# Kernel tuning notes

Hardware: AMD Instinct MI355X
Metric: run time of the kernel (lower is better)

## Reference

```python
import jax, jax.numpy as jnp
import numpy as np

THRESHOLD = 0.5
NEG_POS_RATIO = 3
ALPHA = 1.0


def cxcy_to_xy(c):
    # (cx,cy,w,h) -> (xmin,ymin,xmax,ymax)
    return jnp.concatenate([c[..., :2] - c[..., 2:] / 2.0,
                            c[..., :2] + c[..., 2:] / 2.0], axis=-1)


def gcxgcy_to_cxcy(g, priors):
    # standard SSD decode with variances (10, 5)
    return jnp.concatenate([g[..., :2] * priors[..., 2:] / 10.0 + priors[..., :2],
                            jnp.exp(g[..., 2:] / 5.0) * priors[..., 2:]], axis=-1)


def jaccard(set1, set2):
    # set1: [n1,4], set2: [n2,4], xyxy -> IoU matrix [n1,n2]
    lo = jnp.maximum(set1[:, None, :2], set2[None, :, :2])
    hi = jnp.minimum(set1[:, None, 2:], set2[None, :, 2:])
    wh = jnp.clip(hi - lo, 0.0)
    inter = wh[..., 0] * wh[..., 1]
    a1 = (set1[:, 2] - set1[:, 0]) * (set1[:, 3] - set1[:, 1])
    a2 = (set2[:, 2] - set2[:, 0]) * (set2[:, 3] - set2[:, 1])
    return inter / (a1[:, None] + a2[None, :] - inter)


def match_one(b, l, priors_xy):
    # b: [n_obj,4] GT boxes, l: [n_obj] labels, priors_xy: [P,4]
    n_obj = b.shape[0]
    ov = jaccard(b, priors_xy)                      # [n_obj, P]
    obj_for_prior = jnp.argmax(ov, axis=0)          # [P]
    ov_for_prior = jnp.max(ov, axis=0)              # [P]
    prior_for_obj = jnp.argmax(ov, axis=1)          # [n_obj]
    # force each object to own its best prior
    obj_for_prior = obj_for_prior.at[prior_for_obj].set(jnp.arange(n_obj))
    ov_for_prior = ov_for_prior.at[prior_for_obj].set(1.0)
    lab = l[obj_for_prior]
    lab = jnp.where(ov_for_prior < THRESHOLD, 0, lab)
    return lab, b[obj_for_prior]


def ciou(b1, b2):
    # elementwise CIoU over [..., 4] xyxy boxes -> [...]
    w1 = b1[..., 2] - b1[..., 0]; h1 = b1[..., 3] - b1[..., 1]
    w2 = b2[..., 2] - b2[..., 0]; h2 = b2[..., 3] - b2[..., 1]
    area1 = w1 * h1; area2 = w2 * h2
    cx1 = (b1[..., 2] + b1[..., 0]) / 2; cy1 = (b1[..., 3] + b1[..., 1]) / 2
    cx2 = (b2[..., 2] + b2[..., 0]) / 2; cy2 = (b2[..., 3] + b2[..., 1]) / 2
    in_wh = jnp.clip(jnp.minimum(b1[..., 2:], b2[..., 2:]) - jnp.maximum(b1[..., :2], b2[..., :2]), 0.0)
    out_wh = jnp.clip(jnp.maximum(b1[..., 2:], b2[..., 2:]) - jnp.minimum(b1[..., :2], b2[..., :2]), 0.0)
    inner_diag = (cx2 - cx1) ** 2 + (cy2 - cy1) ** 2
    outer_diag = out_wh[..., 0] ** 2 + out_wh[..., 1] ** 2
    inner = in_wh[..., 0] * in_wh[..., 1]
    iou = inner / (area1 + area2 - inner)
    v = (4.0 / (np.pi ** 2)) * (jnp.arctan(w2 / h2) - jnp.arctan(w1 / h1)) ** 2
    alpha = jax.lax.stop_gradient(v / (1.0 - iou + v))  # torch.no_grad()
    return 1.0 - iou + inner_diag / outer_diag + alpha * v


def setup_inputs() -> dict:
    key = jax.random.key(0)
    ks = jax.random.split(key, 7)
    N, P, C, NOBJ = 32, 8732, 81, 24
    predicted_locs = jax.random.normal(ks[0], (N, P, 4), jnp.float32)
    predicted_scores = jax.random.normal(ks[1], (N, P, C), jnp.float32)
    mins = jax.random.uniform(ks[2], (N, NOBJ, 2), minval=0.0, maxval=0.7)
    sizes = jax.random.uniform(ks[3], (N, NOBJ, 2), minval=0.05, maxval=0.3)
    boxes = jnp.concatenate([mins, mins + sizes], axis=-1)  # well-formed xyxy
    labels = jax.random.randint(ks[4], (N, NOBJ), 1, C)      # 1..C-1 (0 = background)
    pc = jax.random.uniform(ks[5], (P, 2), minval=0.05, maxval=0.95)
    pwh = jax.random.uniform(ks[6], (P, 2), minval=0.05, maxval=0.5)
    priors_cxcy = jnp.concatenate([pc, pwh], axis=-1)
    return {"predicted_locs": predicted_locs, "predicted_scores": predicted_scores,
            "boxes": boxes, "labels": labels, "priors_cxcy": priors_cxcy}


def reference(predicted_locs, predicted_scores, boxes, labels, priors_cxcy):
    priors_xy = cxcy_to_xy(priors_cxcy)
    # per-image GT->prior matching (vectorized over batch)
    true_classes, decoded_true = jax.vmap(match_one, in_axes=(0, 0, None))(boxes, labels, priors_xy)
    decoded_pred = cxcy_to_xy(gcxgcy_to_cxcy(predicted_locs, priors_cxcy[None]))  # [N,P,4]
    pos = true_classes != 0                              # [N,P]
    posf = pos.astype(predicted_locs.dtype)
    n_pos_total = jnp.sum(posf)
    # localization: CIoU mean over positive priors
    loc_loss = jnp.sum(ciou(decoded_pred, decoded_true) * posf) / n_pos_total
    # confidence: CE per prior
    logp = jax.nn.log_softmax(predicted_scores, axis=-1)
    conf_all = -jnp.take_along_axis(logp, true_classes[..., None], axis=-1)[..., 0]  # [N,P]
    conf_pos_sum = jnp.sum(conf_all * posf)
    # hard negative mining: top (neg_pos_ratio * n_pos) negatives per image
    conf_neg = jnp.where(pos, 0.0, conf_all)
    conf_neg_sorted = -jnp.sort(-conf_neg, axis=1)       # descending
    n_hard = NEG_POS_RATIO * jnp.sum(pos, axis=1)        # [N]
    ranks = jnp.arange(conf_neg_sorted.shape[1])[None, :]
    hard_mask = (ranks < n_hard[:, None]).astype(conf_all.dtype)
    conf_hard_neg_sum = jnp.sum(conf_neg_sorted * hard_mask)
    conf_loss = (conf_hard_neg_sum + conf_pos_sum) / n_pos_total
    return conf_loss + ALPHA * loc_loss
```

## Files before the change

### kernel.cpp

```cpp
#include <hip/hip_runtime.h>
#include <math.h>

#define BLK  256
#define BLKM 1024

constexpr int N_IMG = 32;
constexpr int P_PRI = 8732;
constexpr int C_CLS = 81;
constexpr int N_OBJ = 24;
constexpr int RPB   = 64;
constexpr int PB2   = (P_PRI + RPB - 1) / RPB;
constexpr int NBLK2 = PB2 * N_IMG;
constexpr int LROW  = 84;
constexpr int NLD   = 6;

__global__ void k_obj_match(const float* __restrict__ boxes,
                            const float* __restrict__ priors,
                            int* __restrict__ prior_for_obj,
                            int* __restrict__ npos) {
    const int o = blockIdx.x;
    const int n = blockIdx.y;
    const int tid = threadIdx.x;

    if (o == 0 && tid == 0) npos[n] = 0;

    const float x1 = boxes[(n * N_OBJ + o) * 4 + 0];
    const float y1 = boxes[(n * N_OBJ + o) * 4 + 1];
    const float x2 = boxes[(n * N_OBJ + o) * 4 + 2];
    const float y2 = boxes[(n * N_OBJ + o) * 4 + 3];
    const float ab = (x2 - x1) * (y2 - y1);

    const float4* pr4 = (const float4*)priors;

    float bv = -1.0f;
    int   bi = P_PRI;
    for (int p = tid; p < P_PRI; p += BLK) {
        const float4 c = pr4[p];
        const float px1 = c.x - c.z / 2.0f, py1 = c.y - c.w / 2.0f;
        const float px2 = c.x + c.z / 2.0f, py2 = c.y + c.w / 2.0f;
        const float pa  = (px2 - px1) * (py2 - py1);
        const float lox = fmaxf(x1, px1), loy = fmaxf(y1, py1);
        const float hix = fminf(x2, px2), hiy = fminf(y2, py2);
        const float iw = fmaxf(hix - lox, 0.0f), ih = fmaxf(hiy - loy, 0.0f);
        const float inter = iw * ih;
        const float iou = inter / (ab + pa - inter);
        if (iou > bv) { bv = iou; bi = p; }
    }

    __shared__ float sv[BLK];
    __shared__ int   si[BLK];
    sv[tid] = bv; si[tid] = bi;
    __syncthreads();
    for (int s = BLK / 2; s > 0; s >>= 1) {
        if (tid < s) {
            const float v2 = sv[tid + s]; const int i2 = si[tid + s];
            if (v2 > sv[tid] || (v2 == sv[tid] && i2 < si[tid])) { sv[tid] = v2; si[tid] = i2; }
        }
        __syncthreads();
    }
    if (tid == 0) prior_for_obj[n * N_OBJ + o] = si[0];
}

__global__ void __launch_bounds__(BLK, 7)
k_main(const float* __restrict__ locs,
       const float* __restrict__ scores,
       const float* __restrict__ boxes,
       const int*   __restrict__ labels,
       const float* __restrict__ priors,
       const int*   __restrict__ prior_for_obj,
       float* __restrict__ conf_neg,
       int*   __restrict__ npos,
       float* __restrict__ partial_conf,
       float* __restrict__ partial_loc) {
    __shared__ float sdata[RPB * LROW];
    __shared__ int   pfo[N_OBJ];
    __shared__ int   slab[N_OBJ];
    __shared__ float wred[4][4];

    const int n   = blockIdx.y;
    const int r0  = blockIdx.x * RPB;
    const int tid = threadIdx.x;
    const int rows = min(RPB, P_PRI - r0);
    const int nvec = (rows * C_CLS) >> 2;

    const float4* src = (const float4*)(scores + ((size_t)n * P_PRI + r0) * C_CLS);
    float4 ld[NLD];
#pragma unroll
    for (int k = 0; k < NLD; ++k) {
        const int i = tid + k * BLK;
        if (i < nvec) ld[k] = src[i];
    }

    if (tid < N_OBJ) pfo[tid] = prior_for_obj[n * N_OBJ + tid];
    if (tid >= 64 && tid < 64 + N_OBJ) slab[tid - 64] = labels[n * N_OBJ + (tid - 64)];

    const int row = tid >> 2;
    const int q   = tid & 3;
    const int p   = r0 + row;
    const int psafe = (p < P_PRI) ? p : (P_PRI - 1);
    const float4 c = ((const float4*)priors)[psafe];
    const float px1 = c.x - c.z / 2.0f, py1 = c.y - c.w / 2.0f;
    const float px2 = c.x + c.z / 2.0f, py2 = c.y + c.w / 2.0f;
    const float pa  = (px2 - px1) * (py2 - py1);

    const float4* bxg = (const float4*)(boxes + (size_t)n * N_OBJ * 4);
    float bv = -1.0f;
    int   bo = q * 6;
#pragma unroll
    for (int j = 0; j < 6; ++j) {
        const int o = q * 6 + j;
        const float4 b = bxg[o];
        const float lox = fmaxf(b.x, px1), loy = fmaxf(b.y, py1);
        const float hix = fminf(b.z, px2), hiy = fminf(b.w, py2);
        const float iw = fmaxf(hix - lox, 0.0f), ih = fmaxf(hiy - loy, 0.0f);
        const float inter = iw * ih;
        const float ab = (b.z - b.x) * (b.w - b.y);
        const float iou = inter / (ab + pa - inter);
        if (iou > bv) { bv = iou; bo = o; }
    }
#pragma unroll
    for (int m = 1; m < 4; m <<= 1) {
        const float v2 = __shfl_xor(bv, m);
        const int   o2 = __shfl_xor(bo, m);
        if (v2 > bv || (v2 == bv && o2 < bo)) { bv = v2; bo = o2; }
    }

#pragma unroll
    for (int k = 0; k < NLD; ++k) {
        const int i = tid + k * BLK;
        if (i < nvec) {
            const int f  = i * 4;
            const int r  = (int)((unsigned)f / 81u);
            const int cc = f - r * 81;
            const int base = r * LROW + cc;
            const float vv[4] = {ld[k].x, ld[k].y, ld[k].z, ld[k].w};
#pragma unroll
            for (int j = 0; j < 4; ++j) {
                int a = base + j;
                if (cc + j >= 81) a += (LROW - C_CLS);
                sdata[a] = vv[j];
            }
        }
    }
    __syncthreads();

    int fo = -1;
#pragma unroll
    for (int j = 0; j < 6; ++j) {
        const int o = q * 6 + j;
        if (pfo[o] == p) fo = o;
    }
#pragma unroll
    for (int m = 1; m < 4; m <<= 1) fo = max(fo, __shfl_xor(fo, m));

    int   obj = (fo >= 0) ? fo : bo;
    float ov  = (fo >= 0) ? 1.0f : bv;

    float s = 0.0f;
    const float* rbase = sdata + row * LROW;
    if (row < rows) {
        const float4* rv = (const float4*)(rbase + 20 * q);
        float a0 = 0.0f, a1 = 0.0f;
#pragma unroll
        for (int i = 0; i < 5; ++i) {
            const float4 v = rv[i];
            a0 += __expf(v.x) + __expf(v.y);
            a1 += __expf(v.z) + __expf(v.w);
        }
        s = a0 + a1;
        if (q == 3) s += __expf(rbase[80]);
    }
    s += __shfl_xor(s, 1);
    s += __shfl_xor(s, 2);

    int cls = slab[obj];
    if (ov < 0.5f) cls = 0;

    float confpos = 0.0f, locv = 0.0f;
    int   cnt1 = 0;
    if (q == 0 && row < rows) {
        const float conf = __logf(s) - rbase[cls];
        const bool pos = (cls != 0);
        conf_neg[n * P_PRI + p] = pos ? 0.0f : fmaxf(conf, 0.0f);
        if (pos) {
            cnt1 = 1;
            confpos = conf;
            const float4 g = ((const float4*)locs)[(size_t)n * P_PRI + p];
            const float cx = g.x * c.z / 10.0f + c.x;
            const float cy = g.y * c.w / 10.0f + c.y;
            const float w  = expf(g.z / 5.0f) * c.z;
            const float hh = expf(g.w / 5.0f) * c.w;
            const float b1x1 = cx - w / 2.0f, b1y1 = cy - hh / 2.0f;
            const float b1x2 = cx + w / 2.0f, b1y2 = cy + hh / 2.0f;

            const float4 tb = bxg[obj];
            const float w1 = b1x2 - b1x1, h1 = b1y2 - b1y1;
            const float w2 = tb.z - tb.x, h2 = tb.w - tb.y;
            const float area1 = w1 * h1,  area2 = w2 * h2;
            const float c1x = (b1x2 + b1x1) / 2.0f, c1y = (b1y2 + b1y1) / 2.0f;
            const float c2x = (tb.z + tb.x) / 2.0f, c2y = (tb.w + tb.y) / 2.0f;
            const float inw = fmaxf(fminf(b1x2, tb.z) - fmaxf(b1x1, tb.x), 0.0f);
            const float inh = fmaxf(fminf(b1y2, tb.w) - fmaxf(b1y1, tb.y), 0.0f);
            const float owd = fmaxf(fmaxf(b1x2, tb.z) - fminf(b1x1, tb.x), 0.0f);
            const float ohd = fmaxf(fmaxf(b1y2, tb.w) - fminf(b1y1, tb.y), 0.0f);
            const float inner_diag = (c2x - c1x) * (c2x - c1x) + (c2y - c1y) * (c2y - c1y);
            const float outer_diag = owd * owd + ohd * ohd;
            const float inner = inw * inh;
            const float iou = inner / (area1 + area2 - inner);
            const float K = 0.40528473456935108577551785283891f;
            const float dat = atanf(w2 / h2) - atanf(w1 / h1);
            const float v = K * dat * dat;
            const float alpha = v / (1.0f - iou + v);
            locv = 1.0f - iou + inner_diag / outer_diag + alpha * v;
        }
    }

#pragma unroll
    for (int off = 32; off > 0; off >>= 1) {
        confpos += __shfl_down(confpos, off);
        locv    += __shfl_down(locv, off);
        cnt1    += __shfl_down(cnt1, off);
    }
    const int wid = tid >> 6;
    if ((tid & 63) == 0) {
        wred[wid][0] = confpos; wred[wid][1] = locv; wred[wid][2] = (float)cnt1;
    }
    __syncthreads();
    if (tid == 0) {
        float a = 0.0f, b = 0.0f, d = 0.0f;
#pragma unroll
        for (int w2 = 0; w2 < 4; ++w2) { a += wred[w2][0]; b += wred[w2][1]; d += wred[w2][2]; }
        const int slot = n * gridDim.x + blockIdx.x;
        partial_conf[slot] = a;
        partial_loc [slot] = b;
        atomicAdd(&npos[n], (int)d);
    }
}

__global__ void __launch_bounds__(BLKM)
k_mine(const float* __restrict__ conf_neg,
       const int*   __restrict__ npos,
       float* __restrict__ hardneg) {
    __shared__ int   wcnt[2][BLKM / 64];
    __shared__ float wsum[BLKM / 64];

    const int n    = blockIdx.x;
    const int tid  = threadIdx.x;
    const int wid  = tid >> 6;
    const int lane = tid & 63;

    unsigned v[9];
#pragma unroll
    for (int k = 0; k < 9; ++k) {
        const int p = tid + k * BLKM;
        v[k] = (p < P_PRI) ? __float_as_uint(conf_neg[n * P_PRI + p]) : 0u;
    }

    int k0 = 3 * npos[n];
    if (k0 > P_PRI) k0 = P_PRI;
    if (k0 <= 0) { if (tid == 0) hardneg[n] = 0.0f; return; }

    unsigned prefix = 0u;
    int kk = k0;
    for (int bit = 30; bit >= 0; --bit) {
        const unsigned hi = (prefix >> bit) | 1u;
        int cnt = 0;
#pragma unroll
        for (int k = 0; k < 9; ++k)
            cnt += __popcll(__ballot((v[k] >> bit) == hi));
        if (lane == 0) wcnt[bit & 1][wid] = cnt;
        __syncthreads();
        int tot = 0;
#pragma unroll
        for (int w = 0; w < BLKM / 64; ++w) tot += wcnt[bit & 1][w];
        if (tot >= kk) prefix |= (1u << bit);
        else           kk -= tot;
    }

    float psum = 0.0f; int pcnt = 0;
#pragma unroll
    for (int k = 0; k < 9; ++k) {
        if (v[k] > prefix) { psum += __uint_as_float(v[k]); ++pcnt; }
    }
#pragma unroll
    for (int off = 32; off > 0; off >>= 1) {
        psum += __shfl_down(psum, off);
        pcnt += __shfl_down(pcnt, off);
    }
    __syncthreads();
    if (lane == 0) { wsum[wid] = psum; wcnt[0][wid] = pcnt; }
    __syncthreads();
    if (tid == 0) {
        float S = 0.0f; int C = 0;
#pragma unroll
        for (int w = 0; w < BLKM / 64; ++w) { S += wsum[w]; C += wcnt[0][w]; }
        hardneg[n] = S + (float)(k0 - C) * __uint_as_float(prefix);
    }
}

__global__ void k_final(const float* __restrict__ partial_conf,
                        const float* __restrict__ partial_loc,
                        const int*   __restrict__ npos,
                        const float* __restrict__ hardneg,
                        float* __restrict__ out) {
    __shared__ float s1[BLK], s2[BLK], s3[BLK];
    __shared__ int   si[BLK];
    const int tid = threadIdx.x;

    float c = 0.0f, l = 0.0f, h = 0.0f;
    int np = 0;
    for (int i = tid; i < NBLK2; i += BLK) { c += partial_conf[i]; l += partial_loc[i]; }
    if (tid < N_IMG) { h = hardneg[tid]; np = npos[tid]; }

    s1[tid] = c; s2[tid] = l; s3[tid] = h; si[tid] = np;
    __syncthreads();
    for (int s = BLK / 2; s > 0; s >>= 1) {
        if (tid < s) { s1[tid] += s1[tid + s]; s2[tid] += s2[tid + s];
                       s3[tid] += s3[tid + s]; si[tid] += si[tid + s]; }
        __syncthreads();
    }
    if (tid == 0) {
        const float npt = (float)si[0];
        const float conf_loss = (s3[0] + s1[0]) / npt;
        const float loc_loss  = s2[0] / npt;
        out[0] = conf_loss + loc_loss;
    }
}

extern "C" void kernel_launch(void* const* d_in, const int* in_sizes, int n_in,
                              void* d_out, int out_size, void* d_ws, size_t ws_size,
                              hipStream_t stream) {
    const float* locs   = (const float*)d_in[0];
    const float* scores = (const float*)d_in[1];
    const float* boxes  = (const float*)d_in[2];
    const int*   labels = (const int*)  d_in[3];
    const float* priors = (const float*)d_in[4];
    float* out = (float*)d_out;

    char* w = (char*)d_ws;
    float* conf_neg      = (float*)w; w += (size_t)N_IMG * P_PRI * 4;
    int*   prior_for_obj = (int*)w;   w += (size_t)N_IMG * N_OBJ * 4;
    int*   npos          = (int*)w;   w += (size_t)N_IMG * 4;
    float* partial_conf  = (float*)w; w += (size_t)NBLK2 * 4;
    float* partial_loc   = (float*)w; w += (size_t)NBLK2 * 4;
    float* hardneg       = (float*)w; w += (size_t)N_IMG * 4;

    dim3 gridO(N_OBJ, N_IMG);
    k_obj_match<<<gridO, BLK, 0, stream>>>(boxes, priors, prior_for_obj, npos);

    dim3 gridM(PB2, N_IMG);
    k_main<<<gridM, BLK, 0, stream>>>(locs, scores, boxes, labels, priors,
                                      prior_for_obj, conf_neg, npos,
                                      partial_conf, partial_loc);

    k_mine<<<N_IMG, BLKM, 0, stream>>>(conf_neg, npos, hardneg);

    k_final<<<1, BLK, 0, stream>>>(partial_conf, partial_loc, npos, hardneg, out);
}
```

Measured before the change: 88.44 us.

## Load score rows directly into registers with strided per-thread reads, dropping LDS staging

Replaces the coalesced float4 load of the whole score tile into padded shared memory with each thread reading 20 strided scalars (q + 4*i) of its own row straight from global memory. The logit for the target class is now picked in registers with a compare-select and combined across the 4 lanes with shuffles, instead of being read from LDS. This removes the LDS write/read traffic and the 21.5 KB shared allocation, which should allow more resident blocks, and the launch-bounds occupancy hint is relaxed to match. The cost is less efficient global access: adjacent lanes touch interleaved words of 324-byte rows and issue scalar loads rather than vector ones.

```diff
diff --git a/kernel.cpp b/kernel.cpp
--- a/kernel.cpp
+++ b/kernel.cpp
@@ -11,8 +11,6 @@
 constexpr int RPB   = 64;
 constexpr int PB2   = (P_PRI + RPB - 1) / RPB;
 constexpr int NBLK2 = PB2 * N_IMG;
-constexpr int LROW  = 84;
-constexpr int NLD   = 6;
 
 __global__ void k_obj_match(const float* __restrict__ boxes,
                             const float* __restrict__ priors,
@@ -61,7 +59,7 @@
     if (tid == 0) prior_for_obj[n * N_OBJ + o] = si[0];
 }
 
-__global__ void __launch_bounds__(BLK, 7)
+__global__ void __launch_bounds__(BLK)
 k_main(const float* __restrict__ locs,
        const float* __restrict__ scores,
        const float* __restrict__ boxes,
@@ -72,7 +70,6 @@
        int*   __restrict__ npos,
        float* __restrict__ partial_conf,
        float* __restrict__ partial_loc) {
-    __shared__ float sdata[RPB * LROW];
     __shared__ int   pfo[N_OBJ];
     __shared__ int   slab[N_OBJ];
     __shared__ float wred[4][4];
@@ -81,15 +78,6 @@
     const int r0  = blockIdx.x * RPB;
     const int tid = threadIdx.x;
     const int rows = min(RPB, P_PRI - r0);
-    const int nvec = (rows * C_CLS) >> 2;
-
-    const float4* src = (const float4*)(scores + ((size_t)n * P_PRI + r0) * C_CLS);
-    float4 ld[NLD];
-#pragma unroll
-    for (int k = 0; k < NLD; ++k) {
-        const int i = tid + k * BLK;
-        if (i < nvec) ld[k] = src[i];
-    }
 
     if (tid < N_OBJ) pfo[tid] = prior_for_obj[n * N_OBJ + tid];
     if (tid >= 64 && tid < 64 + N_OBJ) slab[tid - 64] = labels[n * N_OBJ + (tid - 64)];
@@ -98,6 +86,14 @@
     const int q   = tid & 3;
     const int p   = r0 + row;
     const int psafe = (p < P_PRI) ? p : (P_PRI - 1);
+
+    const float* xrow = scores + (size_t)(n * P_PRI + psafe) * C_CLS;
+    float v[20];
+#pragma unroll
+    for (int i = 0; i < 20; ++i) v[i] = xrow[q + 4 * i];
+    float v80 = 0.0f;
+    if (q == 0) v80 = xrow[80];
+
     const float4 c = ((const float4*)priors)[psafe];
     const float px1 = c.x - c.z / 2.0f, py1 = c.y - c.w / 2.0f;
     const float px2 = c.x + c.z / 2.0f, py2 = c.y + c.w / 2.0f;
@@ -124,24 +120,6 @@
         const int   o2 = __shfl_xor(bo, m);
         if (v2 > bv || (v2 == bv && o2 < bo)) { bv = v2; bo = o2; }
     }
-
-#pragma unroll
-    for (int k = 0; k < NLD; ++k) {
-        const int i = tid + k * BLK;
-        if (i < nvec) {
-            const int f  = i * 4;
-            const int r  = (int)((unsigned)f / 81u);
-            const int cc = f - r * 81;
-            const int base = r * LROW + cc;
-            const float vv[4] = {ld[k].x, ld[k].y, ld[k].z, ld[k].w};
-#pragma unroll
-            for (int j = 0; j < 4; ++j) {
-                int a = base + j;
-                if (cc + j >= 81) a += (LROW - C_CLS);
-                sdata[a] = vv[j];
-            }
-        }
-    }
     __syncthreads();
 
     int fo = -1;
@@ -153,33 +131,34 @@
 #pragma unroll
     for (int m = 1; m < 4; m <<= 1) fo = max(fo, __shfl_xor(fo, m));
 
-    int   obj = (fo >= 0) ? fo : bo;
-    float ov  = (fo >= 0) ? 1.0f : bv;
-
-    float s = 0.0f;
-    const float* rbase = sdata + row * LROW;
-    if (row < rows) {
-        const float4* rv = (const float4*)(rbase + 20 * q);
-        float a0 = 0.0f, a1 = 0.0f;
-#pragma unroll
-        for (int i = 0; i < 5; ++i) {
-            const float4 v = rv[i];
-            a0 += __expf(v.x) + __expf(v.y);
-            a1 += __expf(v.z) + __expf(v.w);
-        }
-        s = a0 + a1;
-        if (q == 3) s += __expf(rbase[80]);
-    }
-    s += __shfl_xor(s, 1);
-    s += __shfl_xor(s, 2);
+    const int   obj = (fo >= 0) ? fo : bo;
+    const float ov  = (fo >= 0) ? 1.0f : bv;
 
     int cls = slab[obj];
     if (ov < 0.5f) cls = 0;
+
+    float a0 = 0.0f, a1 = 0.0f, sel = 0.0f;
+#pragma unroll
+    for (int i = 0; i < 20; ++i) {
+        const int cc = q + 4 * i;
+        const float e = __expf(v[i]);
+        if (i & 1) a1 += e; else a0 += e;
+        sel += (cc == cls) ? v[i] : 0.0f;
+    }
+    float s = a0 + a1;
+    if (q == 0) {
+        s += __expf(v80);
+        sel += (cls == 80) ? v80 : 0.0f;
+    }
+    s   += __shfl_xor(s, 1);
+    s   += __shfl_xor(s, 2);
+    sel += __shfl_xor(sel, 1);
+    sel += __shfl_xor(sel, 2);
 
     float confpos = 0.0f, locv = 0.0f;
     int   cnt1 = 0;
     if (q == 0 && row < rows) {
-        const float conf = __logf(s) - rbase[cls];
+        const float conf = __logf(s) - sel;
         const bool pos = (cls != 0);
         conf_neg[n * P_PRI + p] = pos ? 0.0f : fmaxf(conf, 0.0f);
         if (pos) {
@@ -209,9 +188,9 @@
             const float iou = inner / (area1 + area2 - inner);
             const float K = 0.40528473456935108577551785283891f;
             const float dat = atanf(w2 / h2) - atanf(w1 / h1);
-            const float v = K * dat * dat;
-            const float alpha = v / (1.0f - iou + v);
-            locv = 1.0f - iou + inner_diag / outer_diag + alpha * v;
+            const float vv = K * dat * dat;
+            const float alpha = vv / (1.0f - iou + vv);
+            locv = 1.0f - iou + inner_diag / outer_diag + alpha * vv;
         }
     }
 
```

Measured after the change: 86.03 us. 2.7% less time.
